# Kernel optimization log

Measured on AMD Instinct MI355X. Metric: run time of the kernel, lower is better.

Reference implementation:

```python
import jax, jax.numpy as jnp
import numpy as np


def setup_inputs() -> dict:
    key = jax.random.key(0)
    k0, k1, k2, k3 = jax.random.split(key, 4)
    T, B, K, L, DEG = 2000, 2048, 64, 64, 3
    return {
        "currents": jax.random.normal(k0, (T, B), dtype=jnp.float32),
        "a": jax.random.normal(k1, (K,), dtype=jnp.float32) * 0.05,
        "b_lag": jax.random.normal(k2, (L,), dtype=jnp.float32) * 1e-3,
        "poly_coeff": jax.random.normal(k3, (1, DEG + 1), dtype=jnp.float32) * 0.3,
        "b_act": jnp.zeros((1,), dtype=jnp.float32),
        "max_current": jnp.full((1,), 100.0, dtype=jnp.float32),
        "max_firing_rate": jnp.full((1,), 100.0, dtype=jnp.float32),
    }


def _poly_act(z, poly_coeff, b_act, max_current, max_firing_rate):
    # PolynomialActivation.forward: x=(z-b)/max_current; poly=sum_d x^d * coeff_d^2
    x = (z - b_act[0]) / max_current[0]  # [B]
    deg = poly_coeff.shape[1] - 1
    coeff = (poly_coeff ** 2)[0]  # [deg+1]
    # build integer powers safely (negative bases) via repeated multiply
    pows = [jnp.ones_like(x)]
    for _ in range(deg):
        pows.append(pows[-1] * x)
    powers = jnp.stack(pows, axis=-1)  # [B, deg+1]
    poly = powers @ coeff  # [B]
    return jax.nn.relu(max_firing_rate[0] * jnp.tanh(poly))


def reference(currents, a, b_lag, poly_coeff, b_act, max_current, max_firing_rate):
    T, B = currents.shape
    K, L = a.shape[0], b_lag.shape[0]

    def step(carry, c_t):
        cur_buf, fs_buf = carry  # [B,K], [B,L]
        cur_buf = jnp.concatenate([cur_buf[:, 1:], c_t[:, None]], axis=1)
        x = cur_buf @ a                      # einsum('j,ij->i')
        y = 1000.0 * (fs_buf @ b_lag)        # einsum('j,ij->i')
        f = _poly_act(x + y, poly_coeff, b_act, max_current, max_firing_rate)
        fs_buf = jnp.concatenate([fs_buf[:, 1:], f[:, None]], axis=1)
        return (cur_buf, fs_buf), f

    init = (jnp.zeros((B, K), currents.dtype), jnp.zeros((B, L), currents.dtype))
    _, fs = jax.lax.scan(step, init, currents)  # fs: [T, B]
    return fs
```

## Files before the change

### kernel.cpp

```cpp
#include <hip/hip_runtime.h>

#define T_STEPS 2000
#define BATCH   2048

__global__ __launch_bounds__(256) void fused_kernel(
    const float* __restrict__ currents, const float* __restrict__ a,
    const float* __restrict__ b_lag, const float* __restrict__ poly_coeff,
    const float* __restrict__ b_act, const float* __restrict__ max_current,
    const float* __restrict__ max_firing_rate, float* __restrict__ out)
{
    int tid  = threadIdx.x;
    int lane = tid & 63;
    int wid  = tid >> 6;
    int b    = blockIdx.x * 4 + wid;

    float inv = 1.0f / max_current[0];
    float cba = -b_act[0] * inv;
    float af  = a[63 - lane] * inv;
    float gam = (1000.0f * inv) * b_lag[63 - lane];

    const float K2 = 2.8853900817779268f;
    float c0 = poly_coeff[0], c1 = poly_coeff[1], c2 = poly_coeff[2], c3 = poly_coeff[3];
    float k0 = K2 * c0 * c0, k1 = K2 * c1 * c1, k2 = K2 * c2 * c2, k3 = K2 * c3 * c3;
    float M  = max_firing_rate[0];
    float m2 = -2.0f * M;

    auto bcast = [](float v, int l) {
        return __builtin_bit_cast(float,
            __builtin_amdgcn_readlane(__builtin_bit_cast(int, v), l));
    };
    auto rotl1 = [](float v) {
        int i = __builtin_bit_cast(int, v);
        return __builtin_bit_cast(float,
            __builtin_amdgcn_update_dpp(i, i, 0x134, 0xf, 0xf, false));
    };

    const float* ccol   = currents + b;
    float*       outcol = out + b;

    float R  = cba;
    float cv = ccol[(long)lane * BATCH];
    float fv = 0.0f;

    auto step = [&](int s) {
        float c = bcast(cv, s);
        R = fmaf(af, c, R);
        float u = bcast(R, 0);
        float u2 = u * u;
        float a1 = fmaf(u, k1, k0);
        float a2 = fmaf(u, k3, k2);
        float p  = fmaf(u2, a2, a1);
        float e  = __builtin_amdgcn_exp2f(p);
        float r  = __builtin_amdgcn_rcpf(e + 1.0f);
        float f  = fmaxf(fmaf(m2, r, M), 0.0f);
        float Rr = rotl1(R);
        Rr = (lane == 63) ? cba : Rr;
        R  = fmaf(gam, f, Rr);
        fv = (lane == s) ? f : fv;
    };

    for (int chunk = 0; chunk < 31; ++chunk) {
        int t0 = chunk * 64;
        int tp = t0 + 64 + lane;
        float cv_next = (tp < T_STEPS) ? ccol[(long)tp * BATCH] : 0.0f;
#pragma unroll
        for (int s = 0; s < 64; ++s) step(s);
        outcol[(long)(t0 + lane) * BATCH] = fv;
        cv = cv_next;
    }
#pragma unroll
    for (int s = 0; s < 16; ++s) step(s);
    if (lane < 16) outcol[(long)(1984 + lane) * BATCH] = fv;
}

extern "C" void kernel_launch(void* const* d_in, const int* in_sizes, int n_in,
                              void* d_out, int out_size, void* d_ws, size_t ws_size,
                              hipStream_t stream) {
    const float* currents   = (const float*)d_in[0];
    const float* a          = (const float*)d_in[1];
    const float* b_lag      = (const float*)d_in[2];
    const float* poly_coeff = (const float*)d_in[3];
    const float* b_act      = (const float*)d_in[4];
    const float* mc         = (const float*)d_in[5];
    const float* mfr        = (const float*)d_in[6];
    float* out = (float*)d_out;

    fused_kernel<<<BATCH / 4, 256, 0, stream>>>(
        currents, a, b_lag, poly_coeff, b_act, mc, mfr, out);
}
```

Measured before the change: 211.2 us.

## Replace DPP shift with rotating-index accumulator and rational tanh approximation

Each lane now stays fixed and the step index rotates, using per-lane coefficient tables preloaded from shared memory into 64 register pairs. This removes the per-step DPP rotate and its lane-63 fixup. The exp2+rcp tanh is replaced by a clamped Padé-style rational polynomial that needs one rcp. The large register table and the added occupancy hint risk register pressure or spills. The rational form is only an approximation of tanh and is clamped at 5.

```diff
diff --git a/kernel.cpp b/kernel.cpp
--- a/kernel.cpp
+++ b/kernel.cpp
@@ -3,74 +3,90 @@
 #define T_STEPS 2000
 #define BATCH   2048
 
-__global__ __launch_bounds__(256) void fused_kernel(
+#define FORCE_VGPR(x) asm("" : "+v"(x))
+
+__global__ __launch_bounds__(256, 2) void fused_kernel(
     const float* __restrict__ currents, const float* __restrict__ a,
     const float* __restrict__ b_lag, const float* __restrict__ poly_coeff,
     const float* __restrict__ b_act, const float* __restrict__ max_current,
     const float* __restrict__ max_firing_rate, float* __restrict__ out)
 {
+    __shared__ float2 stab[64];
     int tid  = threadIdx.x;
     int lane = tid & 63;
     int wid  = tid >> 6;
     int b    = blockIdx.x * 4 + wid;
 
     float inv = 1.0f / max_current[0];
+    if (tid < 64) {
+        float2 v;
+        v.x = a[63 - tid] * inv;
+        v.y = (1000.0f * inv) * b_lag[(64 - tid) & 63];
+        stab[tid] = v;
+    }
+    __syncthreads();
+
+    float2 tab[64];
+#pragma unroll
+    for (int s = 0; s < 64; ++s) tab[s] = stab[(lane - s) & 63];
+
     float cba = -b_act[0] * inv;
-    float af  = a[63 - lane] * inv;
-    float gam = (1000.0f * inv) * b_lag[63 - lane];
 
-    const float K2 = 2.8853900817779268f;
     float c0 = poly_coeff[0], c1 = poly_coeff[1], c2 = poly_coeff[2], c3 = poly_coeff[3];
-    float k0 = K2 * c0 * c0, k1 = K2 * c1 * c1, k2 = K2 * c2 * c2, k3 = K2 * c3 * c3;
+    float k0 = c0 * c0, k1 = c1 * c1, k2 = c2 * c2, k3 = c3 * c3;
     float M  = max_firing_rate[0];
-    float m2 = -2.0f * M;
+    float N0 = 135135.0f * M, N1 = 17325.0f * M, N2 = 378.0f * M;
+    float D0 = 135135.0f, D1 = 62370.0f, D2 = 3150.0f, D3 = 28.0f;
+
+    FORCE_VGPR(cba);
+    FORCE_VGPR(k0); FORCE_VGPR(k1); FORCE_VGPR(k2); FORCE_VGPR(k3);
+    FORCE_VGPR(M);  FORCE_VGPR(N0); FORCE_VGPR(N1); FORCE_VGPR(N2);
+    FORCE_VGPR(D0); FORCE_VGPR(D1); FORCE_VGPR(D2); FORCE_VGPR(D3);
 
     auto bcast = [](float v, int l) {
         return __builtin_bit_cast(float,
             __builtin_amdgcn_readlane(__builtin_bit_cast(int, v), l));
-    };
-    auto rotl1 = [](float v) {
-        int i = __builtin_bit_cast(int, v);
-        return __builtin_bit_cast(float,
-            __builtin_amdgcn_update_dpp(i, i, 0x134, 0xf, 0xf, false));
     };
 
     const float* ccol   = currents + b;
     float*       outcol = out + b;
 
     float R  = cba;
+    float F  = 0.0f;
     float cv = ccol[(long)lane * BATCH];
-    float fv = 0.0f;
 
     auto step = [&](int s) {
         float c = bcast(cv, s);
-        R = fmaf(af, c, R);
-        float u = bcast(R, 0);
+        R = fmaf(tab[s].x, c, R);
+        float u = bcast(R, s);
         float u2 = u * u;
         float a1 = fmaf(u, k1, k0);
         float a2 = fmaf(u, k3, k2);
         float p  = fmaf(u2, a2, a1);
-        float e  = __builtin_amdgcn_exp2f(p);
-        float r  = __builtin_amdgcn_rcpf(e + 1.0f);
-        float f  = fmaxf(fmaf(m2, r, M), 0.0f);
-        float Rr = rotl1(R);
-        Rr = (lane == 63) ? cba : Rr;
-        R  = fmaf(gam, f, Rr);
-        fv = (lane == s) ? f : fv;
+        float q  = __builtin_amdgcn_fmed3f(p, 0.0f, 5.0f);
+        float w  = q * q;
+        float N  = fmaf(w, fmaf(w, fmaf(w, M,  N2), N1), N0);
+        float D  = fmaf(w, fmaf(w, fmaf(w, D3, D2), D1), D0);
+        float r  = __builtin_amdgcn_rcpf(D);
+        float f  = (q * N) * r;
+        bool own = (lane == s);
+        R = own ? cba : R;
+        R = fmaf(tab[s].y, f, R);
+        F = own ? f : F;
     };
 
     for (int chunk = 0; chunk < 31; ++chunk) {
-        int t0 = chunk * 64;
-        int tp = t0 + 64 + lane;
-        float cv_next = (tp < T_STEPS) ? ccol[(long)tp * BATCH] : 0.0f;
+        long t0 = (long)chunk * 64;
+        long tp = t0 + 64 + lane;
+        float cvn = (tp < T_STEPS) ? ccol[tp * BATCH] : 0.0f;
 #pragma unroll
         for (int s = 0; s < 64; ++s) step(s);
-        outcol[(long)(t0 + lane) * BATCH] = fv;
-        cv = cv_next;
+        outcol[(t0 + lane) * BATCH] = F;
+        cv = cvn;
     }
 #pragma unroll
     for (int s = 0; s < 16; ++s) step(s);
-    if (lane < 16) outcol[(long)(1984 + lane) * BATCH] = fv;
+    if (lane < 16) outcol[(long)(1984 + lane) * BATCH] = F;
 }
 
 extern "C" void kernel_launch(void* const* d_in, const int* in_sizes, int n_in,
```

Measured after the change: 227.7 us. 1.08x slower.
